# Kernel optimization log

Measured on AMD Instinct MI355X. Metric: run time of the kernel, lower is better.

The kernel has to match this reference:

```python
import jax, jax.numpy as jnp
import numpy as np

B, D, H, W, K = 2, 128, 256, 256, 4
OFFSET_SCALE = 1.0
BN_EPS = 1e-5


def conv2d(x, w, b=None, pad='SAME'):
    y = jax.lax.conv_general_dilated(x, w, (1, 1), pad,
                                     dimension_numbers=('NCHW', 'OIHW', 'NCHW'))
    if b is not None:
        y = y + b[None, :, None, None]
    return y


def grid_sample_border(img, gx, gy):
    # img: (b,d,H,W); gx,gy: (b,K,H,W) normalized coords in [-1,1]
    # bilinear, padding_mode='border', align_corners=True
    b, d, h, w = img.shape
    x = jnp.clip((gx + 1.0) * 0.5 * (w - 1), 0.0, w - 1)
    y = jnp.clip((gy + 1.0) * 0.5 * (h - 1), 0.0, h - 1)
    x0f = jnp.floor(x); y0f = jnp.floor(y)
    wx = x - x0f; wy = y - y0f
    x0 = x0f.astype(jnp.int32); y0 = y0f.astype(jnp.int32)
    x1 = jnp.minimum(x0 + 1, w - 1); y1 = jnp.minimum(y0 + 1, h - 1)
    imgT = jnp.transpose(img, (0, 2, 3, 1))  # (b,H,W,d)
    bidx = jnp.arange(b)[:, None, None, None]  # broadcasts over (b,K,H,W)
    def gather(yi, xi):
        return imgT[bidx, yi, xi]  # (b,K,H,W,d)
    out = (gather(y0, x0) * ((1 - wx) * (1 - wy))[..., None]
           + gather(y0, x1) * (wx * (1 - wy))[..., None]
           + gather(y1, x0) * ((1 - wx) * wy)[..., None]
           + gather(y1, x1) * (wx * wy)[..., None])
    return out  # (b,K,H,W,d)


def setup_inputs() -> dict:
    key = jax.random.key(0)
    ks = jax.random.split(key, 6)
    return {
        'bev': jax.random.normal(ks[0], (B, D, H, W), jnp.float32),
        'offset_w': jax.random.normal(ks[1], (2 * K, D, 3, 3), jnp.float32) * 0.02,
        'offset_b': jax.random.normal(ks[2], (2 * K,), jnp.float32) * 0.02,
        'weight_w': jax.random.normal(ks[3], (K, D, 3, 3), jnp.float32) * 0.05,
        'weight_b': jnp.zeros((K,), jnp.float32),
        'proj_w': jax.random.normal(ks[4], (D, D, 1, 1), jnp.float32) * (1.0 / np.sqrt(D)),
        'bn_gamma': jnp.ones((D,), jnp.float32),
        'bn_beta': jnp.zeros((D,), jnp.float32),
    }


def reference(bev, offset_w, offset_b, weight_w, weight_b, proj_w, bn_gamma, bn_beta):
    b, d, h, w = bev.shape
    # per-pixel K offsets (pixels) and K attention weights
    offsets = conv2d(bev, offset_w, offset_b) * OFFSET_SCALE  # (b,2K,H,W)
    w_logits = conv2d(bev, weight_w, weight_b)                # (b,K,H,W)
    attn = jax.nn.softmax(w_logits, axis=1)                   # softmax over K
    # base grid: replicates torch meshgrid(xy) + transpose (requires H==W)
    xs = jnp.linspace(-1.0, 1.0, w)
    ys = jnp.linspace(-1.0, 1.0, h)
    base_x = xs[:, None] * jnp.ones((1, h), jnp.float32)  # base_x[i,j] = xs[i]
    base_y = jnp.ones((w, 1), jnp.float32) * ys[None, :]  # base_y[i,j] = ys[j]
    off = offsets.reshape(b, K, 2, h, w)
    dx = off[:, :, 0]  # (b,K,H,W)
    dy = off[:, :, 1]
    dx_n = dx * (2.0 / (w - 1)) if w > 1 else dx * 0.0
    dy_n = dy * (2.0 / (h - 1)) if h > 1 else dy * 0.0
    gx = base_x[None, None] + dx_n  # (b,K,H,W)
    gy = base_y[None, None] + dy_n
    sampled = grid_sample_border(bev, gx, gy)  # (b,K,H,W,d)
    aggregated = jnp.einsum('bkhwd,bkhw->bdhw', sampled, attn)
    # proj: 1x1 conv (no bias) + BatchNorm2d (training mode: batch stats) + GELU(exact)
    y = conv2d(aggregated, proj_w)
    mean = jnp.mean(y, axis=(0, 2, 3), keepdims=True)
    var = jnp.mean((y - mean) ** 2, axis=(0, 2, 3), keepdims=True)
    y = (y - mean) * jax.lax.rsqrt(var + BN_EPS)
    y = y * bn_gamma[None, :, None, None] + bn_beta[None, :, None, None]
    return jax.nn.gelu(y, approximate=False)
```

## Files before the change

kernel.cpp:

```cpp
#include <hip/hip_runtime.h>
#include <math.h>

#define BB 2
#define DD 128
#define HH 256
#define WW 256
#define KK 4
#define HWC (HH*WW)
#define SROW2 320

typedef unsigned int u32;
typedef unsigned short ushort;
typedef __attribute__((ext_vector_type(8))) short bf16x8;
typedef __attribute__((ext_vector_type(4))) float f32x4;

#define OA_OFF    0
#define WTT_OFF   1572864
#define WP_OFF    1589248
#define STATS_OFF 1603072
#define PART_OFF  1603392
#define BEVT_OFF  1605440
#define PACC_OFF  18382656
#define PART2_OFF PACC_OFF
#define WBF_OFF   26771264
#define WCB_OFF   26779456
#define WS_NEED_BEVT  ((size_t)PACC_OFF * 4)
#define WS_NEED_FULL3 ((size_t)(WCB_OFF + 9216) * 4)

__device__ __forceinline__ u32 f2bf(float x) {
    u32 u = __builtin_bit_cast(u32, x);
    return (u + 0x7fffu + ((u >> 16) & 1u)) >> 16;
}
__device__ __forceinline__ u32 pkbf(float a, float b) {
    return f2bf(a) | (f2bf(b) << 16);
}
__device__ __forceinline__ float bflo(u32 d) { return __builtin_bit_cast(float, d << 16); }
__device__ __forceinline__ float bfhi(u32 d) { return __builtin_bit_cast(float, d & 0xffff0000u); }

__global__ __launch_bounds__(256) void k0_prep(
    const float* __restrict__ projw, const float* __restrict__ offw,
    const float* __restrict__ wtw, float* __restrict__ wtT, float* __restrict__ wp)
{
    int idx = blockIdx.x * 256 + threadIdx.x;
    if (idx < 16384) {
        int d = idx >> 7, o = idx & 127;
        wtT[d * 128 + o] = projw[o * 128 + d];
    }
    if (idx < 13824) {
        int c = idx / 108; int r = idx % 108; int o = r / 9; int t = r % 9;
        wp[idx] = (o < 8) ? offw[(o*128 + c)*9 + t] : wtw[((o-8)*128 + c)*9 + t];
    }
}

__global__ __launch_bounds__(256) void k0bc(
    const float* __restrict__ projw, const float* __restrict__ offw,
    const float* __restrict__ wtw, ushort* __restrict__ wbf,
    ushort* __restrict__ wcb)
{
    int idx = blockIdx.x * 256 + threadIdx.x;
    if (idx < 16384) wbf[idx] = (ushort)f2bf(projw[idx]);
    if (idx < 18432) {
        int tap = idx >> 11;
        int rem = idx & 2047;
        int oo = rem >> 7, c = rem & 127;
        float v = 0.f;
        if (oo < 8)       v = offw[(oo*128 + c)*9 + tap];
        else if (oo < 12) v = wtw[((oo-8)*128 + c)*9 + tap];
        wcb[idx] = (ushort)f2bf(v);
    }
}

__global__ __launch_bounds__(256) void k2t_bf(
    const float* __restrict__ bev, ushort* __restrict__ bevtb)
{
    __shared__ float T[64 * 128];
    int tid = threadIdx.x;
    int bidx = blockIdx.x;
    int b = bidx >> 10;
    int rem = bidx & 1023;
    int yrow = rem >> 2;
    int x0 = (rem & 3) << 6;

    const float* src = bev + ((size_t)b * DD) * HWC + (size_t)yrow * WW + x0;
    #pragma unroll 4
    for (int k = 0; k < 32; k++) {
        int flat = k * 256 + tid;
        int d = flat >> 6, xl = flat & 63;
        float v = src[(size_t)d * HWC + xl];
        T[xl * 128 + (((d >> 2) ^ (xl & 31)) << 2) + (d & 3)] = v;
    }
    __syncthreads();
    ushort* dst = bevtb + (((size_t)b * HH + yrow) * WW + x0) * 128;
    #pragma unroll 4
    for (int k = 0; k < 8; k++) {
        int flat = k * 256 + tid;
        int d4 = flat & 31, xl = (flat >> 5) & 63;
        float4 v = *(const float4*)&T[xl * 128 + ((d4 ^ (xl & 31)) << 2)];
        uint2 pk;
        pk.x = pkbf(v.x, v.y);
        pk.y = pkbf(v.z, v.w);
        *(uint2*)(dst + (size_t)xl * 128 + (d4 << 2)) = pk;
    }
}

__global__ __launch_bounds__(128) void k1m_conv_mfma(
    const ushort* __restrict__ bevtb, const ushort* __restrict__ wcb,
    const float* __restrict__ offb, const float* __restrict__ wtb,
    float* __restrict__ oa)
{
    __shared__ uint4 lds4[1632];

    int tid = threadIdx.x;
    int wv = tid >> 6;
    int l = tid & 63;
    int lm = l & 15, lk = l >> 4;
    int wgid = blockIdx.x;
    int lin = (wgid & 7) * 512 + (wgid >> 3);
    int b = lin >> 11;
    int i = (lin >> 3) & 255;
    int jt = lin & 7;
    int x0 = jt * 32;

    const ushort* bb = bevtb + (size_t)b * HWC * 128;
    for (int z = tid; z < 1632; z += 128) {
        int row = z / 544;
        int rem = z - row * 544;
        int pl = rem >> 4;
        int q  = rem & 15;
        int yy = i - 1 + row;
        int x  = x0 - 1 + pl;
        bool ok = ((unsigned)yy < HH) && ((unsigned)x < WW);
        uint4 v = make_uint4(0u, 0u, 0u, 0u);
        if (ok) v = *(const uint4*)(bb + ((size_t)(yy * WW + x) << 7) + q * 8);
        lds4[row * 544 + pl * 16 + (q ^ (pl & 15))] = v;
    }
    __syncthreads();

    f32x4 acc = (f32x4)(0.f);
    #pragma unroll
    for (int dy = 0; dy < 3; dy++) {
        #pragma unroll
        for (int dx = 0; dx < 3; dx++) {
            int pl = wv * 16 + lm + dx;
            const uint4* bp = &lds4[dy * 544 + pl * 16];
            int sx = pl & 15;
            const ushort* ap = wcb + (size_t)((dy*3 + dx) * 16 + lm) * 128 + lk * 8;
            #pragma unroll
            for (int kk = 0; kk < 4; kk++) {
                bf16x8 bfr = *(const bf16x8*)&bp[(kk*4 + lk) ^ sx];
                bf16x8 afr = *(const bf16x8*)(ap + kk * 32);
                acc = __builtin_amdgcn_mfma_f32_16x16x32_bf16(afr, bfr, acc, 0, 0, 0);
            }
        }
    }

    float v[4];
    #pragma unroll
    for (int r = 0; r < 4; r++) v[r] = acc[r];

    int j = x0 + wv * 16 + lm;
    if (lk < 2) {
        #pragma unroll
        for (int r = 0; r < 4; r++) v[r] += offb[lk*4 + r];
    } else if (lk == 2) {
        float l4[4];
        #pragma unroll
        for (int r = 0; r < 4; r++) l4[r] = v[r] + wtb[r];
        float m = fmaxf(fmaxf(l4[0], l4[1]), fmaxf(l4[2], l4[3]));
        float e[4]; float se = 0.f;
        #pragma unroll
        for (int r = 0; r < 4; r++) { e[r] = expf(l4[r] - m); se += e[r]; }
        float inv = 1.f / se;
        #pragma unroll
        for (int r = 0; r < 4; r++) v[r] = e[r] * inv;
    }
    if (lk < 3) {
        size_t basep = (size_t)b * 12 * HWC + (size_t)i * WW + j;
        #pragma unroll
        for (int r = 0; r < 4; r++)
            oa[basep + (size_t)(lk*4 + r) * HWC] = v[r];
    }
}

#define TAPPTR(t) (bt + ((size_t)((((t) & 1) ? (pa[(t) >> 1] >> 16) : (pa[(t) >> 1] & 0xffffu))) << 7))
#define FMA8(S, V, W) do { \
    S[0] = fmaf(W, bflo((V).x), S[0]); S[1] = fmaf(W, bfhi((V).x), S[1]); \
    S[2] = fmaf(W, bflo((V).y), S[2]); S[3] = fmaf(W, bfhi((V).y), S[3]); \
    S[4] = fmaf(W, bflo((V).z), S[4]); S[5] = fmaf(W, bfhi((V).z), S[5]); \
    S[6] = fmaf(W, bflo((V).w), S[6]); S[7] = fmaf(W, bfhi((V).w), S[7]); \
} while (0)

__global__ __launch_bounds__(256, 4) void k2f_sample_proj(
    const ushort* __restrict__ bevtb, const float* __restrict__ oa,
    const ushort* __restrict__ wbf, float* __restrict__ y,
    float* __restrict__ part2)
{
    __shared__ uint4 P[32 * 16];

    int tid = threadIdx.x;
    int wgid = blockIdx.x;
    int lin = (wgid & 7) * 512 + (wgid >> 3);
    int b = lin >> 11;
    int pix0 = (lin & 2047) << 5;

    int q8 = tid & 7;
    int pixl = tid >> 3;
    int pix = pix0 + pixl;
    int p = pix >> 8;
    int q = pix & 255;

    const float* ob = oa + (size_t)b * 12 * HWC + (size_t)p * WW + q;
    unsigned pa[8]; float cw[16];
    #pragma unroll
    for (int k = 0; k < 4; k++) {
        float dx = ob[(size_t)(2*k)   * HWC];
        float dy = ob[(size_t)(2*k+1) * HWC];
        float a  = ob[(size_t)(8+k)   * HWC];
        float x  = fminf(fmaxf((float)p + dx, 0.f), (float)(WW-1));
        float yv = fminf(fmaxf((float)q + dy, 0.f), (float)(HH-1));
        float x0f = floorf(x); float y0f = floorf(yv);
        int x0 = (int)x0f; int y0 = (int)y0f;
        int x1 = min(x0 + 1, WW - 1); int y1 = min(y0 + 1, HH - 1);
        float wx = x - x0f; float wy = yv - y0f;
        pa[k*2+0] = (unsigned)(y0*WW + x0) | ((unsigned)(y0*WW + x1) << 16);
        pa[k*2+1] = (unsigned)(y1*WW + x0) | ((unsigned)(y1*WW + x1) << 16);
        cw[k*4+0] = a * (1.f - wx) * (1.f - wy);
        cw[k*4+1] = a * wx * (1.f - wy);
        cw[k*4+2] = a * (1.f - wx) * wy;
        cw[k*4+3] = a * wx * wy;
    }

    const ushort* bt = bevtb + (size_t)b * HWC * 128 + q8 * 8;

    float s[2][8];
    #pragma unroll
    for (int c = 0; c < 2; c++)
        #pragma unroll
        for (int e = 0; e < 8; e++) s[c][e] = 0.f;

    uint4 L0[8], L1[8];
    #pragma unroll
    for (int t = 0; t < 8; t++) L0[t] = *(const uint4*)(TAPPTR(t));
    #pragma unroll
    for (int t = 0; t < 8; t++) L1[t] = *(const uint4*)(TAPPTR(t + 8));
    #pragma unroll
    for (int t = 0; t < 8; t++) {
        uint4 v = L0[t];
        L0[t] = *(const uint4*)(TAPPTR(t) + 64);
        FMA8(s[0], v, cw[t]);
    }
    #pragma unroll
    for (int t = 0; t < 8; t++) {
        uint4 v = L1[t];
        L1[t] = *(const uint4*)(TAPPTR(t + 8) + 64);
        FMA8(s[0], v, cw[t + 8]);
    }
    #pragma unroll
    for (int t = 0; t < 8; t++) FMA8(s[1], L0[t], cw[t]);
    #pragma unroll
    for (int t = 0; t < 8; t++) FMA8(s[1], L1[t], cw[t + 8]);

    int sxr = pixl & 15;
    #pragma unroll
    for (int c = 0; c < 2; c++) {
        uint4 pk;
        pk.x = pkbf(s[c][0], s[c][1]);
        pk.y = pkbf(s[c][2], s[c][3]);
        pk.z = pkbf(s[c][4], s[c][5]);
        pk.w = pkbf(s[c][6], s[c][7]);
        P[pixl * 16 + ((c * 8 + q8) ^ sxr)] = pk;
    }
    __syncthreads();

    int wv = tid >> 6;
    int l = tid & 63;
    int lm = l & 15, lk = l >> 4;
    int o0 = wv << 5;

    f32x4 acc[2][2];
    #pragma unroll
    for (int ot = 0; ot < 2; ot++)
        #pragma unroll
        for (int nt = 0; nt < 2; nt++)
            acc[ot][nt] = (f32x4)(0.f);

    #pragma unroll
    for (int ot = 0; ot < 2; ot++) {
        const ushort* ap = wbf + (size_t)(o0 + ot * 16 + lm) * 128 + lk * 8;
        bf16x8 a4[4];
        #pragma unroll
        for (int kk = 0; kk < 4; kk++)
            a4[kk] = *(const bf16x8*)(ap + kk * 32);
        #pragma unroll
        for (int nt = 0; nt < 2; nt++) {
            int row = nt * 16 + lm;
            #pragma unroll
            for (int kk = 0; kk < 4; kk++) {
                bf16x8 bfr = *(const bf16x8*)&P[row * 16 + ((kk * 4 + lk) ^ lm)];
                acc[ot][nt] = __builtin_amdgcn_mfma_f32_16x16x32_bf16(
                    a4[kk], bfr, acc[ot][nt], 0, 0, 0);
            }
        }
    }

    #pragma unroll
    for (int ot = 0; ot < 2; ot++)
        #pragma unroll
        for (int nt = 0; nt < 2; nt++)
            #pragma unroll
            for (int r = 0; r < 4; r++)
                y[((size_t)b * DD + o0 + ot * 16 + lk * 4 + r) * HWC + pix0 + nt * 16 + lm]
                    = acc[ot][nt][r];

    float sm[2][4], sq[2][4];
    #pragma unroll
    for (int ot = 0; ot < 2; ot++)
        #pragma unroll
        for (int r = 0; r < 4; r++) { sm[ot][r] = 0.f; sq[ot][r] = 0.f; }
    #pragma unroll
    for (int ot = 0; ot < 2; ot++)
        #pragma unroll
        for (int nt = 0; nt < 2; nt++)
            #pragma unroll
            for (int r = 0; r < 4; r++) {
                float v = acc[ot][nt][r];
                sm[ot][r] += v;
                sq[ot][r] = fmaf(v, v, sq[ot][r]);
            }
    #pragma unroll
    for (int m = 1; m < 16; m <<= 1) {
        #pragma unroll
        for (int ot = 0; ot < 2; ot++)
            #pragma unroll
            for (int r = 0; r < 4; r++) {
                sm[ot][r] += __shfl_xor(sm[ot][r], m);
                sq[ot][r] += __shfl_xor(sq[ot][r], m);
            }
    }
    if (lm == 0) {
        float* pw = part2 + (size_t)wgid * 256;
        #pragma unroll
        for (int ot = 0; ot < 2; ot++)
            #pragma unroll
            for (int r = 0; r < 4; r++) {
                int o = o0 + ot * 16 + lk * 4 + r;
                pw[o] = sm[ot][r];
                pw[128 + o] = sq[ot][r];
            }
    }
}

__global__ __launch_bounds__(256) void k3b_finalize2(
    const float* __restrict__ part2, const float* __restrict__ gamma,
    const float* __restrict__ beta, float* __restrict__ stats)
{
    int o = blockIdx.x; int tid = threadIdx.x;
    double s = 0.0, s2 = 0.0;
    for (int w = tid; w < 4096; w += 256) {
        s  += (double)part2[(size_t)w * 256 + o];
        s2 += (double)part2[(size_t)w * 256 + 128 + o];
    }
    __shared__ double ls[256], ls2[256];
    ls[tid] = s; ls2[tid] = s2;
    __syncthreads();
    for (int off = 128; off > 0; off >>= 1) {
        if (tid < off) { ls[tid] += ls[tid+off]; ls2[tid] += ls2[tid+off]; }
        __syncthreads();
    }
    if (tid == 0) {
        double N = (double)(BB * HWC);
        double mean = ls[0] / N;
        double var = ls2[0] / N - mean * mean;
        double invs = 1.0 / sqrt(var + 1e-5);
        double g = (double)gamma[o];
        stats[o*2]   = (float)(g * invs);
        stats[o*2+1] = (float)((double)beta[o] - mean * g * invs);
    }
}

__global__ __launch_bounds__(256) void k1_convs(
    const float* __restrict__ bev, const float* __restrict__ wp,
    const float* __restrict__ offb, const float* __restrict__ wtb,
    float* __restrict__ oa)
{
    __shared__ float rows[2][3][260];
    int tid = threadIdx.x;
    int p = blockIdx.x;
    int b = p / HH; int i = p % HH; int j = tid;
    const float* bb = bev + (size_t)b * DD * HWC;

    if (tid < 12) { int bf = tid / 6, r = tid % 6; rows[bf][r >> 1][(r & 1) ? 257 : 0] = 0.f; }
    #pragma unroll
    for (int l = 0; l < 3; l++) {
        int yy = i + l - 1;
        rows[0][l][1 + tid] = ((unsigned)yy < HH) ? bb[yy * WW + tid] : 0.f;
    }
    __syncthreads();

    float acc[12];
    #pragma unroll
    for (int o = 0; o < 12; o++) acc[o] = 0.f;

    for (int c = 0; c < 128; c++) {
        int cb = c & 1, nb = cb ^ 1;
        float rv[3];
        if (c < 127) {
            const float* pln = bb + (size_t)(c + 1) * HWC;
            #pragma unroll
            for (int l = 0; l < 3; l++) {
                int yy = i + l - 1;
                rv[l] = ((unsigned)yy < HH) ? pln[yy * WW + tid] : 0.f;
            }
        }
        float v[9];
        #pragma unroll
        for (int dy = 0; dy < 3; dy++)
            #pragma unroll
            for (int dx = 0; dx < 3; dx++)
                v[dy*3 + dx] = rows[cb][dy][tid + dx];
        const float* wc = wp + c * 108;
        #pragma unroll
        for (int o = 0; o < 12; o++) {
            float s = acc[o];
            #pragma unroll
            for (int t = 0; t < 9; t++) s = fmaf(wc[o*9 + t], v[t], s);
            acc[o] = s;
        }
        if (c < 127) {
            #pragma unroll
            for (int l = 0; l < 3; l++) rows[nb][l][1 + tid] = rv[l];
        }
        __syncthreads();
    }

    float outv[12];
    #pragma unroll
    for (int o = 0; o < 8; o++) outv[o] = acc[o] + offb[o];
    float l4[4];
    #pragma unroll
    for (int k = 0; k < 4; k++) l4[k] = acc[8+k] + wtb[k];
    float m = fmaxf(fmaxf(l4[0], l4[1]), fmaxf(l4[2], l4[3]));
    float e[4]; float se = 0.f;
    #pragma unroll
    for (int k = 0; k < 4; k++) { e[k] = expf(l4[k] - m); se += e[k]; }
    float inv = 1.f / se;
    #pragma unroll
    for (int k = 0; k < 4; k++) outv[8+k] = e[k] * inv;

    size_t basep = (size_t)b * 12 * HWC + (size_t)i * WW + j;
    #pragma unroll
    for (int o = 0; o < 12; o++) oa[basep + (size_t)o * HWC] = outv[o];
}

__global__ __launch_bounds__(256) void k2t_transpose(
    const float* __restrict__ bev, float* __restrict__ bevt)
{
    __shared__ float T[64 * 128];
    int tid = threadIdx.x;
    int bidx = blockIdx.x;
    int b = bidx >> 10;
    int rem = bidx & 1023;
    int yrow = rem >> 2;
    int x0 = (rem & 3) << 6;

    const float* src = bev + ((size_t)b * DD) * HWC + (size_t)yrow * WW + x0;
    #pragma unroll 4
    for (int k = 0; k < 32; k++) {
        int flat = k * 256 + tid;
        int d = flat >> 6, xl = flat & 63;
        float v = src[(size_t)d * HWC + xl];
        T[xl * 128 + (((d >> 2) ^ (xl & 31)) << 2) + (d & 3)] = v;
    }
    __syncthreads();
    float* dst = bevt + (((size_t)b * HH + yrow) * WW + x0) * 128;
    #pragma unroll 4
    for (int k = 0; k < 8; k++) {
        int flat = k * 256 + tid;
        int d4 = flat & 31, xl = (flat >> 5) & 63;
        float4 v = *(const float4*)&T[xl * 128 + ((d4 ^ (xl & 31)) << 2)];
        *(float4*)(dst + (size_t)xl * 128 + (d4 << 2)) = v;
    }
}

__global__ __launch_bounds__(512, 2) void k2_sample_proj_t(
    const float* __restrict__ bevt, const float* __restrict__ oa,
    const float* __restrict__ wt, float* __restrict__ y)
{
    __shared__ float S[2][16 * SROW2];

    int tid = threadIdx.x;
    int bidx = blockIdx.x;
    int b  = bidx >> 8;
    int p0 = ((bidx >> 4) & 15) * 16;
    int q0 = (bidx & 15) * 16;

    int gpix = tid >> 1;
    int gp = gpix & 15;
    int gq = gpix >> 4;
    int dgrp = tid & 1;
    int swr = gp * 20 + gq;

    int wv = tid >> 6;
    int wvu = __builtin_amdgcn_readfirstlane(wv);
    int lane = tid & 63;
    int lp = lane >> 2;
    int q4 = (lane & 3) << 2;
    int soff = lp * 20 + q4;

    const float* ob = oa + (size_t)b * 12 * HWC + (size_t)(p0 + gp) * WW + (q0 + gq);
    unsigned pa[8]; float cw[16];
    #pragma unroll
    for (int k = 0; k < 4; k++) {
        float dx = ob[(size_t)(2*k)   * HWC];
        float dy = ob[(size_t)(2*k+1) * HWC];
        float a  = ob[(size_t)(8+k)   * HWC];
        float x  = fminf(fmaxf((float)(p0 + gp) + dx, 0.f), (float)(WW-1));
        float yv = fminf(fmaxf((float)(q0 + gq) + dy, 0.f), (float)(HH-1));
        float x0f = floorf(x); float y0f = floorf(yv);
        int x0 = (int)x0f; int y0 = (int)y0f;
        int x1 = min(x0 + 1, WW - 1); int y1 = min(y0 + 1, HH - 1);
        float wx = x - x0f; float wy = yv - y0f;
        pa[k*2+0] = (unsigned)(y0*WW + x0) | ((unsigned)(y0*WW + x1) << 16);
        pa[k*2+1] = (unsigned)(y1*WW + x0) | ((unsigned)(y1*WW + x1) << 16);
        cw[k*4+0] = a * (1.f - wx) * (1.f - wy);
        cw[k*4+1] = a * wx * (1.f - wy);
        cw[k*4+2] = a * (1.f - wx) * wy;
        cw[k*4+3] = a * wx * wy;
    }

    const float* bt = bevt + (size_t)b * HWC * 128 + dgrp * 8;

    float acc[64];
    #pragma unroll
    for (int t = 0; t < 64; t++) acc[t] = 0.f;

    {
        float4 s0 = make_float4(0,0,0,0), s1 = make_float4(0,0,0,0);
        #pragma unroll
        for (int t = 0; t < 16; t++) {
            unsigned pix = (t & 1) ? (pa[t >> 1] >> 16) : (pa[t >> 1] & 0xffffu);
            const float4* tp = (const float4*)(bt + ((size_t)pix << 7));
            float4 va = tp[0], vb = tp[1];
            float c = cw[t];
            s0.x = fmaf(c, va.x, s0.x); s0.y = fmaf(c, va.y, s0.y);
            s0.z = fmaf(c, va.z, s0.z); s0.w = fmaf(c, va.w, s0.w);
            s1.x = fmaf(c, vb.x, s1.x); s1.y = fmaf(c, vb.y, s1.y);
            s1.z = fmaf(c, vb.z, s1.z); s1.w = fmaf(c, vb.w, s1.w);
        }
        int r = dgrp * 8;
        S[0][(r+0)*SROW2 + swr] = s0.x; S[0][(r+1)*SROW2 + swr] = s0.y;
        S[0][(r+2)*SROW2 + swr] = s0.z; S[0][(r+3)*SROW2 + swr] = s0.w;
        S[0][(r+4)*SROW2 + swr] = s1.x; S[0][(r+5)*SROW2 + swr] = s1.y;
        S[0][(r+6)*SROW2 + swr] = s1.z; S[0][(r+7)*SROW2 + swr] = s1.w;
    }
    __syncthreads();

    for (int c = 0; c < 8; c++) {
        int cur = c & 1;
        const float* Sc = &S[cur][0];
        float* Sn = &S[cur ^ 1][0];
        int d0 = c * 16;
        int dn = d0 + 16;
        bool more = (c < 7);

        float4 g0 = make_float4(0,0,0,0), g1 = make_float4(0,0,0,0);
        float4 pf0, pf1;
        if (more) {
            unsigned pix = pa[0] & 0xffffu;
            const float4* tp = (const float4*)(bt + ((size_t)pix << 7) + dn);
            pf0 = tp[0]; pf1 = tp[1];
        }

        #pragma unroll
        for (int dl = 0; dl < 16; dl++) {
            float4 cur0 = pf0, cur1 = pf1;
            if (more && dl < 15) {
                int t = dl + 1;
                unsigned pix = (t & 1) ? (pa[t >> 1] >> 16) : (pa[t >> 1] & 0xffffu);
                const float4* tp = (const float4*)(bt + ((size_t)pix << 7) + dn);
                pf0 = tp[0]; pf1 = tp[1];
            }

            float4 sv = *(const float4*)(Sc + dl * SROW2 + soff);
            const float4* wq = (const float4*)(wt + (size_t)(d0 + dl) * 128 + wvu * 16);
            #pragma unroll
            for (int oi4 = 0; oi4 < 4; oi4++) {
                float4 w4 = wq[oi4];
                int ob4 = oi4 * 16;
                acc[ob4+ 0] = fmaf(w4.x, sv.x, acc[ob4+ 0]);
                acc[ob4+ 1] = fmaf(w4.x, sv.y, acc[ob4+ 1]);
                acc[ob4+ 2] = fmaf(w4.x, sv.z, acc[ob4+ 2]);
                acc[ob4+ 3] = fmaf(w4.x, sv.w, acc[ob4+ 3]);
                acc[ob4+ 4] = fmaf(w4.y, sv.x, acc[ob4+ 4]);
                acc[ob4+ 5] = fmaf(w4.y, sv.y, acc[ob4+ 5]);
                acc[ob4+ 6] = fmaf(w4.y, sv.z, acc[ob4+ 6]);
                acc[ob4+ 7] = fmaf(w4.y, sv.w, acc[ob4+ 7]);
                acc[ob4+ 8] = fmaf(w4.z, sv.x, acc[ob4+ 8]);
                acc[ob4+ 9] = fmaf(w4.z, sv.y, acc[ob4+ 9]);
                acc[ob4+10] = fmaf(w4.z, sv.z, acc[ob4+10]);
                acc[ob4+11] = fmaf(w4.z, sv.w, acc[ob4+11]);
                acc[ob4+12] = fmaf(w4.w, sv.x, acc[ob4+12]);
                acc[ob4+13] = fmaf(w4.w, sv.y, acc[ob4+13]);
                acc[ob4+14] = fmaf(w4.w, sv.z, acc[ob4+14]);
                acc[ob4+15] = fmaf(w4.w, sv.w, acc[ob4+15]);
            }

            if (more) {
                float cwt = cw[dl];
                g0.x = fmaf(cwt, cur0.x, g0.x); g0.y = fmaf(cwt, cur0.y, g0.y);
                g0.z = fmaf(cwt, cur0.z, g0.z); g0.w = fmaf(cwt, cur0.w, g0.w);
                g1.x = fmaf(cwt, cur1.x, g1.x); g1.y = fmaf(cwt, cur1.y, g1.y);
                g1.z = fmaf(cwt, cur1.z, g1.z); g1.w = fmaf(cwt, cur1.w, g1.w);
            }
        }

        if (more) {
            int r = dgrp * 8;
            Sn[(r+0)*SROW2 + swr] = g0.x; Sn[(r+1)*SROW2 + swr] = g0.y;
            Sn[(r+2)*SROW2 + swr] = g0.z; Sn[(r+3)*SROW2 + swr] = g0.w;
            Sn[(r+4)*SROW2 + swr] = g1.x; Sn[(r+5)*SROW2 + swr] = g1.y;
            Sn[(r+6)*SROW2 + swr] = g1.z; Sn[(r+7)*SROW2 + swr] = g1.w;
        }
        __syncthreads();
    }

    size_t base = (size_t)b * DD * HWC + (size_t)(p0 + lp) * WW + (q0 + q4);
    #pragma unroll
    for (int oi = 0; oi < 16; oi++) {
        int o = wv * 16 + oi;
        float4 v = make_float4(acc[oi*4+0], acc[oi*4+1], acc[oi*4+2], acc[oi*4+3]);
        *(float4*)(y + base + (size_t)o * HWC) = v;
    }
}

__global__ __launch_bounds__(512, 2) void k2_sample_proj(
    const float* __restrict__ bev, const float* __restrict__ oa,
    const float* __restrict__ wt, float* __restrict__ y)
{
    __shared__ float S[2][16 * SROW2];
    int tid = threadIdx.x;
    int bidx = blockIdx.x;
    int b  = bidx >> 8;
    int p0 = ((bidx >> 4) & 15) * 16;
    int q0 = (bidx & 15) * 16;
    int pix = tid & 255;
    int gq = pix >> 4;
    int gp = pix & 15;
    int dgrp = tid >> 8;
    int swr = gp * 20 + gq;
    int wv = tid >> 6;
    int wvu = __builtin_amdgcn_readfirstlane(wv);
    int lane = tid & 63;
    int lp = lane >> 2;
    int q4 = (lane & 3) << 2;
    int soff = lp * 20 + q4;

    const float* ob = oa + (size_t)b * 12 * HWC + (size_t)(p0 + gp) * WW + (q0 + gq);
    unsigned pa[8]; float cw[16];
    #pragma unroll
    for (int k = 0; k < 4; k++) {
        float dx = ob[(size_t)(2*k)   * HWC];
        float dy = ob[(size_t)(2*k+1) * HWC];
        float a  = ob[(size_t)(8+k)   * HWC];
        float x  = fminf(fmaxf((float)(p0 + gp) + dx, 0.f), (float)(WW-1));
        float yv = fminf(fmaxf((float)(q0 + gq) + dy, 0.f), (float)(HH-1));
        float x0f = floorf(x); float y0f = floorf(yv);
        int x0 = (int)x0f; int y0 = (int)y0f;
        int x1 = min(x0 + 1, WW - 1); int y1 = min(y0 + 1, HH - 1);
        float wx = x - x0f; float wy = yv - y0f;
        pa[k*2+0] = (unsigned)(y0*WW + x0) | ((unsigned)(y0*WW + x1) << 16);
        pa[k*2+1] = (unsigned)(y1*WW + x0) | ((unsigned)(y1*WW + x1) << 16);
        cw[k*4+0] = a * (1.f - wx) * (1.f - wy);
        cw[k*4+1] = a * wx * (1.f - wy);
        cw[k*4+2] = a * (1.f - wx) * wy;
        cw[k*4+3] = a * wx * wy;
    }
    const float* bb = bev + (size_t)b * DD * HWC;
    float acc[64];
    #pragma unroll
    for (int t = 0; t < 64; t++) acc[t] = 0.f;
    #pragma unroll
    for (int dd = 0; dd < 8; dd++) {
        const float* pl = bb + (size_t)(dgrp*8 + dd) * HWC;
        float s = 0.f;
        #pragma unroll
        for (int t = 0; t < 8; t++) {
            unsigned a01 = pa[t];
            s = fmaf(cw[2*t],   pl[a01 & 0xffffu], s);
            s = fmaf(cw[2*t+1], pl[a01 >> 16], s);
        }
        S[0][(dgrp*8 + dd) * SROW2 + swr] = s;
    }
    __syncthreads();
    for (int c = 0; c < 8; c++) {
        int cur = c & 1;
        const float* Sc = &S[cur][0];
        float* Sn = &S[cur ^ 1][0];
        int d0 = c * 16;
        int d0n = d0 + 16;
        bool more = (c < 7);
        #pragma unroll
        for (int dl = 0; dl < 16; dl++) {
            if (dl < 8) {
                if (more) {
                    const float* pl = bb + (size_t)(d0n + dgrp*8 + dl) * HWC;
                    float s = 0.f;
                    #pragma unroll
                    for (int t = 0; t < 8; t++) {
                        unsigned a01 = pa[t];
                        s = fmaf(cw[2*t],   pl[a01 & 0xffffu], s);
                        s = fmaf(cw[2*t+1], pl[a01 >> 16], s);
                    }
                    Sn[(dgrp*8 + dl) * SROW2 + swr] = s;
                }
            }
            float4 sv = *(const float4*)(Sc + dl * SROW2 + soff);
            const float4* wq = (const float4*)(wt + (size_t)(d0 + dl) * 128 + wvu * 16);
            #pragma unroll
            for (int oi4 = 0; oi4 < 4; oi4++) {
                float4 w4 = wq[oi4];
                int ob4 = oi4 * 16;
                acc[ob4+ 0] = fmaf(w4.x, sv.x, acc[ob4+ 0]);
                acc[ob4+ 1] = fmaf(w4.x, sv.y, acc[ob4+ 1]);
                acc[ob4+ 2] = fmaf(w4.x, sv.z, acc[ob4+ 2]);
                acc[ob4+ 3] = fmaf(w4.x, sv.w, acc[ob4+ 3]);
                acc[ob4+ 4] = fmaf(w4.y, sv.x, acc[ob4+ 4]);
                acc[ob4+ 5] = fmaf(w4.y, sv.y, acc[ob4+ 5]);
                acc[ob4+ 6] = fmaf(w4.y, sv.z, acc[ob4+ 6]);
                acc[ob4+ 7] = fmaf(w4.y, sv.w, acc[ob4+ 7]);
                acc[ob4+ 8] = fmaf(w4.z, sv.x, acc[ob4+ 8]);
                acc[ob4+ 9] = fmaf(w4.z, sv.y, acc[ob4+ 9]);
                acc[ob4+10] = fmaf(w4.z, sv.z, acc[ob4+10]);
                acc[ob4+11] = fmaf(w4.z, sv.w, acc[ob4+11]);
                acc[ob4+12] = fmaf(w4.w, sv.x, acc[ob4+12]);
                acc[ob4+13] = fmaf(w4.w, sv.y, acc[ob4+13]);
                acc[ob4+14] = fmaf(w4.w, sv.z, acc[ob4+14]);
                acc[ob4+15] = fmaf(w4.w, sv.w, acc[ob4+15]);
            }
        }
        __syncthreads();
    }
    size_t base = (size_t)b * DD * HWC + (size_t)(p0 + lp) * WW + (q0 + q4);
    #pragma unroll
    for (int oi = 0; oi < 16; oi++) {
        int o = wv * 16 + oi;
        float4 v = make_float4(acc[oi*4+0], acc[oi*4+1], acc[oi*4+2], acc[oi*4+3]);
        *(float4*)(y + base + (size_t)o * HWC) = v;
    }
}

__global__ __launch_bounds__(256) void k3_partial(
    const float* __restrict__ y, double* __restrict__ part)
{
    int blk = blockIdx.x;
    int o = blk >> 2; int sub = blk & 3; int b = sub >> 1; int half = sub & 1;
    const float4* pl = (const float4*)(y + ((size_t)b * DD + o) * HWC + half * (HWC/2));
    int tid = threadIdx.x;
    double s = 0.0, s2 = 0.0;
    for (int idx = tid; idx < HWC/8; idx += 256) {
        float4 v = pl[idx];
        s  += (double)v.x + (double)v.y + (double)v.z + (double)v.w;
        s2 += (double)v.x*v.x + (double)v.y*v.y + (double)v.z*v.z + (double)v.w*v.w;
    }
    __shared__ double ls[256], ls2[256];
    ls[tid] = s; ls2[tid] = s2;
    __syncthreads();
    for (int off = 128; off > 0; off >>= 1) {
        if (tid < off) { ls[tid] += ls[tid+off]; ls2[tid] += ls2[tid+off]; }
        __syncthreads();
    }
    if (tid == 0) { part[blk*2] = ls[0]; part[blk*2+1] = ls2[0]; }
}

__global__ __launch_bounds__(128) void k3_finalize(
    const double* __restrict__ part, const float* __restrict__ gamma,
    const float* __restrict__ beta, float* __restrict__ stats)
{
    int o = threadIdx.x;
    double s = 0.0, s2 = 0.0;
    #pragma unroll
    for (int j = 0; j < 4; j++) { s += part[(o*4+j)*2]; s2 += part[(o*4+j)*2+1]; }
    double N = (double)(BB * HWC);
    double mean = s / N;
    double var = s2 / N - mean * mean;
    double invs = 1.0 / sqrt(var + 1e-5);
    double g = (double)gamma[o];
    stats[o*2]   = (float)(g * invs);
    stats[o*2+1] = (float)((double)beta[o] - mean * g * invs);
}

__global__ __launch_bounds__(256) void k4_bn_gelu(
    float* __restrict__ y, const float* __restrict__ stats)
{
    size_t idx4 = (size_t)blockIdx.x * 256 + threadIdx.x;
    float4* p = (float4*)y;
    float4 v = p[idx4];
    int o = (int)((idx4 * 4) / HWC) % DD;
    float sc = stats[o*2], sh = stats[o*2+1];
    const float inv_sqrt2 = 0.70710678118654752f;
    float g0 = fmaf(v.x, sc, sh);
    float g1 = fmaf(v.y, sc, sh);
    float g2 = fmaf(v.z, sc, sh);
    float g3 = fmaf(v.w, sc, sh);
    v.x = 0.5f * g0 * (1.f + erff(g0 * inv_sqrt2));
    v.y = 0.5f * g1 * (1.f + erff(g1 * inv_sqrt2));
    v.z = 0.5f * g2 * (1.f + erff(g2 * inv_sqrt2));
    v.w = 0.5f * g3 * (1.f + erff(g3 * inv_sqrt2));
    p[idx4] = v;
}

extern "C" void kernel_launch(void* const* d_in, const int* in_sizes, int n_in,
                              void* d_out, int out_size, void* d_ws, size_t ws_size,
                              hipStream_t stream) {
    const float* bev   = (const float*)d_in[0];
    const float* offw  = (const float*)d_in[1];
    const float* offb  = (const float*)d_in[2];
    const float* wtw   = (const float*)d_in[3];
    const float* wtb   = (const float*)d_in[4];
    const float* projw = (const float*)d_in[5];
    const float* gamma = (const float*)d_in[6];
    const float* beta  = (const float*)d_in[7];
    float* out = (float*)d_out;
    float* wsf = (float*)d_ws;

    float* oa    = wsf + OA_OFF;
    float* wtT   = wsf + WTT_OFF;
    float* wp    = wsf + WP_OFF;
    float* stats = wsf + STATS_OFF;
    double* part = (double*)(wsf + PART_OFF);
    float* bevt  = wsf + BEVT_OFF;
    ushort* bevtb = (ushort*)(wsf + BEVT_OFF);
    ushort* wbf  = (ushort*)(wsf + WBF_OFF);
    ushort* wcb  = (ushort*)(wsf + WCB_OFF);
    float* part2 = wsf + PART2_OFF;

    bool full3 = ws_size >= WS_NEED_FULL3;
    bool big   = ws_size >= WS_NEED_BEVT;

    if (full3) {
        hipLaunchKernelGGL(k0bc, dim3(72), dim3(256), 0, stream,
                           projw, offw, wtw, wbf, wcb);
        hipLaunchKernelGGL(k2t_bf, dim3(2048), dim3(256), 0, stream, bev, bevtb);
        hipLaunchKernelGGL(k1m_conv_mfma, dim3(4096), dim3(128), 0, stream,
                           bevtb, wcb, offb, wtb, oa);
        hipLaunchKernelGGL(k2f_sample_proj, dim3(4096), dim3(256), 0, stream,
                           bevtb, oa, wbf, out, part2);
        hipLaunchKernelGGL(k3b_finalize2, dim3(128), dim3(256), 0, stream,
                           part2, gamma, beta, stats);
    } else if (big) {
        hipLaunchKernelGGL(k0_prep, dim3(64), dim3(256), 0, stream,
                           projw, offw, wtw, wtT, wp);
        hipLaunchKernelGGL(k2t_transpose, dim3(2048), dim3(256), 0, stream, bev, bevt);
        hipLaunchKernelGGL(k1_convs, dim3(BB*HH), dim3(256), 0, stream,
                           bev, wp, offb, wtb, oa);
        hipLaunchKernelGGL(k2_sample_proj_t, dim3(BB*256), dim3(512), 0, stream,
                           bevt, oa, wtT, out);
        hipLaunchKernelGGL(k3_partial, dim3(512), dim3(256), 0, stream, out, part);
        hipLaunchKernelGGL(k3_finalize, dim3(1), dim3(128), 0, stream,
                           part, gamma, beta, stats);
    } else {
        hipLaunchKernelGGL(k0_prep, dim3(64), dim3(256), 0, stream,
                           projw, offw, wtw, wtT, wp);
        hipLaunchKernelGGL(k1_convs, dim3(BB*HH), dim3(256), 0, stream,
                           bev, wp, offb, wtb, oa);
        hipLaunchKernelGGL(k2_sample_proj, dim3(BB*256), dim3(512), 0, stream,
                           bev, oa, wtT, out);
        hipLaunchKernelGGL(k3_partial, dim3(512), dim3(256), 0, stream, out, part);
        hipLaunchKernelGGL(k3_finalize, dim3(1), dim3(128), 0, stream,
                           part, gamma, beta, stats);
    }
    hipLaunchKernelGGL(k4_bn_gelu, dim3((BB*DD*HWC)/1024), dim3(256), 0, stream,
                       out, stats);
}
```

Baseline: 156.3 us.

## Store pre-BN projection in bf16 and widen conv tiles to 64 pixels

The sample-projection kernel now writes its pre-BatchNorm output as bf16 into a workspace buffer, and a new BN+GELU kernel reads it in bf16 and writes fp32 output. This halves the write and read traffic of the 16M-element intermediate. The MFMA offset/weight conv kernel now uses 256-thread blocks covering 64 pixels per row, which reuses the halo more and halves the block count. The intermediate fp32 path is also removed. Rounding y to bf16 adds error before normalization, while the batch statistics still come from fp32 accumulators.

```diff
diff --git a/kernel.cpp b/kernel.cpp
--- a/kernel.cpp
+++ b/kernel.cpp
@@ -20,6 +20,7 @@
 #define STATS_OFF 1603072
 #define PART_OFF  1603392
 #define BEVT_OFF  1605440
+#define YBF_OFF   9994048
 #define PACC_OFF  18382656
 #define PART2_OFF PACC_OFF
 #define WBF_OFF   26771264
@@ -103,28 +104,28 @@
     }
 }
 
-__global__ __launch_bounds__(128) void k1m_conv_mfma(
+__global__ __launch_bounds__(256) void k1m_conv_mfma(
     const ushort* __restrict__ bevtb, const ushort* __restrict__ wcb,
     const float* __restrict__ offb, const float* __restrict__ wtb,
     float* __restrict__ oa)
 {
-    __shared__ uint4 lds4[1632];
+    __shared__ uint4 lds4[3168];
 
     int tid = threadIdx.x;
     int wv = tid >> 6;
     int l = tid & 63;
     int lm = l & 15, lk = l >> 4;
     int wgid = blockIdx.x;
-    int lin = (wgid & 7) * 512 + (wgid >> 3);
-    int b = lin >> 11;
-    int i = (lin >> 3) & 255;
-    int jt = lin & 7;
-    int x0 = jt * 32;
+    int lin = (wgid & 7) * 256 + (wgid >> 3);
+    int b = lin >> 10;
+    int i = (lin >> 2) & 255;
+    int jt = lin & 3;
+    int x0 = jt * 64;
 
     const ushort* bb = bevtb + (size_t)b * HWC * 128;
-    for (int z = tid; z < 1632; z += 128) {
-        int row = z / 544;
-        int rem = z - row * 544;
+    for (int z = tid; z < 3168; z += 256) {
+        int row = z / 1056;
+        int rem = z - row * 1056;
         int pl = rem >> 4;
         int q  = rem & 15;
         int yy = i - 1 + row;
@@ -132,7 +133,7 @@
         bool ok = ((unsigned)yy < HH) && ((unsigned)x < WW);
         uint4 v = make_uint4(0u, 0u, 0u, 0u);
         if (ok) v = *(const uint4*)(bb + ((size_t)(yy * WW + x) << 7) + q * 8);
-        lds4[row * 544 + pl * 16 + (q ^ (pl & 15))] = v;
+        lds4[row * 1056 + pl * 16 + (q ^ (pl & 15))] = v;
     }
     __syncthreads();
 
@@ -142,7 +143,7 @@
         #pragma unroll
         for (int dx = 0; dx < 3; dx++) {
             int pl = wv * 16 + lm + dx;
-            const uint4* bp = &lds4[dy * 544 + pl * 16];
+            const uint4* bp = &lds4[dy * 1056 + pl * 16];
             int sx = pl & 15;
             const ushort* ap = wcb + (size_t)((dy*3 + dx) * 16 + lm) * 128 + lk * 8;
             #pragma unroll
@@ -192,7 +193,7 @@
 
 __global__ __launch_bounds__(256, 4) void k2f_sample_proj(
     const ushort* __restrict__ bevtb, const float* __restrict__ oa,
-    const ushort* __restrict__ wbf, float* __restrict__ y,
+    const ushort* __restrict__ wbf, ushort* __restrict__ ybf,
     float* __restrict__ part2)
 {
     __shared__ uint4 P[32 * 16];
@@ -309,8 +310,8 @@
         for (int nt = 0; nt < 2; nt++)
             #pragma unroll
             for (int r = 0; r < 4; r++)
-                y[((size_t)b * DD + o0 + ot * 16 + lk * 4 + r) * HWC + pix0 + nt * 16 + lm]
-                    = acc[ot][nt][r];
+                ybf[((size_t)b * DD + o0 + ot * 16 + lk * 4 + r) * HWC + pix0 + nt * 16 + lm]
+                    = (ushort)f2bf(acc[ot][nt][r]);
 
     float sm[2][4], sq[2][4];
     #pragma unroll
@@ -378,6 +379,33 @@
     }
 }
 
+__global__ __launch_bounds__(256) void k4_bn_gelu_bf(
+    const ushort* __restrict__ ybf, const float* __restrict__ stats,
+    float* __restrict__ out)
+{
+    size_t idx8 = (size_t)blockIdx.x * 256 + threadIdx.x;
+    uint4 v = ((const uint4*)ybf)[idx8];
+    int o = (int)((idx8 * 8) / HWC) % DD;
+    float sc = stats[o*2], sh = stats[o*2+1];
+    const float is2 = 0.70710678118654752f;
+    float g[8];
+    g[0] = fmaf(bflo(v.x), sc, sh); g[1] = fmaf(bfhi(v.x), sc, sh);
+    g[2] = fmaf(bflo(v.y), sc, sh); g[3] = fmaf(bfhi(v.y), sc, sh);
+    g[4] = fmaf(bflo(v.z), sc, sh); g[5] = fmaf(bfhi(v.z), sc, sh);
+    g[6] = fmaf(bflo(v.w), sc, sh); g[7] = fmaf(bfhi(v.w), sc, sh);
+    float4 o0, o1;
+    o0.x = 0.5f * g[0] * (1.f + erff(g[0] * is2));
+    o0.y = 0.5f * g[1] * (1.f + erff(g[1] * is2));
+    o0.z = 0.5f * g[2] * (1.f + erff(g[2] * is2));
+    o0.w = 0.5f * g[3] * (1.f + erff(g[3] * is2));
+    o1.x = 0.5f * g[4] * (1.f + erff(g[4] * is2));
+    o1.y = 0.5f * g[5] * (1.f + erff(g[5] * is2));
+    o1.z = 0.5f * g[6] * (1.f + erff(g[6] * is2));
+    o1.w = 0.5f * g[7] * (1.f + erff(g[7] * is2));
+    ((float4*)out)[idx8 * 2]     = o0;
+    ((float4*)out)[idx8 * 2 + 1] = o1;
+}
+
 __global__ __launch_bounds__(256) void k1_convs(
     const float* __restrict__ bev, const float* __restrict__ wp,
     const float* __restrict__ offb, const float* __restrict__ wtb,
@@ -450,187 +478,6 @@
     size_t basep = (size_t)b * 12 * HWC + (size_t)i * WW + j;
     #pragma unroll
     for (int o = 0; o < 12; o++) oa[basep + (size_t)o * HWC] = outv[o];
-}
-
-__global__ __launch_bounds__(256) void k2t_transpose(
-    const float* __restrict__ bev, float* __restrict__ bevt)
-{
-    __shared__ float T[64 * 128];
-    int tid = threadIdx.x;
-    int bidx = blockIdx.x;
-    int b = bidx >> 10;
-    int rem = bidx & 1023;
-    int yrow = rem >> 2;
-    int x0 = (rem & 3) << 6;
-
-    const float* src = bev + ((size_t)b * DD) * HWC + (size_t)yrow * WW + x0;
-    #pragma unroll 4
-    for (int k = 0; k < 32; k++) {
-        int flat = k * 256 + tid;
-        int d = flat >> 6, xl = flat & 63;
-        float v = src[(size_t)d * HWC + xl];
-        T[xl * 128 + (((d >> 2) ^ (xl & 31)) << 2) + (d & 3)] = v;
-    }
-    __syncthreads();
-    float* dst = bevt + (((size_t)b * HH + yrow) * WW + x0) * 128;
-    #pragma unroll 4
-    for (int k = 0; k < 8; k++) {
-        int flat = k * 256 + tid;
-        int d4 = flat & 31, xl = (flat >> 5) & 63;
-        float4 v = *(const float4*)&T[xl * 128 + ((d4 ^ (xl & 31)) << 2)];
-        *(float4*)(dst + (size_t)xl * 128 + (d4 << 2)) = v;
-    }
-}
-
-__global__ __launch_bounds__(512, 2) void k2_sample_proj_t(
-    const float* __restrict__ bevt, const float* __restrict__ oa,
-    const float* __restrict__ wt, float* __restrict__ y)
-{
-    __shared__ float S[2][16 * SROW2];
-
-    int tid = threadIdx.x;
-    int bidx = blockIdx.x;
-    int b  = bidx >> 8;
-    int p0 = ((bidx >> 4) & 15) * 16;
-    int q0 = (bidx & 15) * 16;
-
-    int gpix = tid >> 1;
-    int gp = gpix & 15;
-    int gq = gpix >> 4;
-    int dgrp = tid & 1;
-    int swr = gp * 20 + gq;
-
-    int wv = tid >> 6;
-    int wvu = __builtin_amdgcn_readfirstlane(wv);
-    int lane = tid & 63;
-    int lp = lane >> 2;
-    int q4 = (lane & 3) << 2;
-    int soff = lp * 20 + q4;
-
-    const float* ob = oa + (size_t)b * 12 * HWC + (size_t)(p0 + gp) * WW + (q0 + gq);
-    unsigned pa[8]; float cw[16];
-    #pragma unroll
-    for (int k = 0; k < 4; k++) {
-        float dx = ob[(size_t)(2*k)   * HWC];
-        float dy = ob[(size_t)(2*k+1) * HWC];
-        float a  = ob[(size_t)(8+k)   * HWC];
-        float x  = fminf(fmaxf((float)(p0 + gp) + dx, 0.f), (float)(WW-1));
-        float yv = fminf(fmaxf((float)(q0 + gq) + dy, 0.f), (float)(HH-1));
-        float x0f = floorf(x); float y0f = floorf(yv);
-        int x0 = (int)x0f; int y0 = (int)y0f;
-        int x1 = min(x0 + 1, WW - 1); int y1 = min(y0 + 1, HH - 1);
-        float wx = x - x0f; float wy = yv - y0f;
-        pa[k*2+0] = (unsigned)(y0*WW + x0) | ((unsigned)(y0*WW + x1) << 16);
-        pa[k*2+1] = (unsigned)(y1*WW + x0) | ((unsigned)(y1*WW + x1) << 16);
-        cw[k*4+0] = a * (1.f - wx) * (1.f - wy);
-        cw[k*4+1] = a * wx * (1.f - wy);
-        cw[k*4+2] = a * (1.f - wx) * wy;
-        cw[k*4+3] = a * wx * wy;
-    }
-
-    const float* bt = bevt + (size_t)b * HWC * 128 + dgrp * 8;
-
-    float acc[64];
-    #pragma unroll
-    for (int t = 0; t < 64; t++) acc[t] = 0.f;
-
-    {
-        float4 s0 = make_float4(0,0,0,0), s1 = make_float4(0,0,0,0);
-        #pragma unroll
-        for (int t = 0; t < 16; t++) {
-            unsigned pix = (t & 1) ? (pa[t >> 1] >> 16) : (pa[t >> 1] & 0xffffu);
-            const float4* tp = (const float4*)(bt + ((size_t)pix << 7));
-            float4 va = tp[0], vb = tp[1];
-            float c = cw[t];
-            s0.x = fmaf(c, va.x, s0.x); s0.y = fmaf(c, va.y, s0.y);
-            s0.z = fmaf(c, va.z, s0.z); s0.w = fmaf(c, va.w, s0.w);
-            s1.x = fmaf(c, vb.x, s1.x); s1.y = fmaf(c, vb.y, s1.y);
-            s1.z = fmaf(c, vb.z, s1.z); s1.w = fmaf(c, vb.w, s1.w);
-        }
-        int r = dgrp * 8;
-        S[0][(r+0)*SROW2 + swr] = s0.x; S[0][(r+1)*SROW2 + swr] = s0.y;
-        S[0][(r+2)*SROW2 + swr] = s0.z; S[0][(r+3)*SROW2 + swr] = s0.w;
-        S[0][(r+4)*SROW2 + swr] = s1.x; S[0][(r+5)*SROW2 + swr] = s1.y;
-        S[0][(r+6)*SROW2 + swr] = s1.z; S[0][(r+7)*SROW2 + swr] = s1.w;
-    }
-    __syncthreads();
-
-    for (int c = 0; c < 8; c++) {
-        int cur = c & 1;
-        const float* Sc = &S[cur][0];
-        float* Sn = &S[cur ^ 1][0];
-        int d0 = c * 16;
-        int dn = d0 + 16;
-        bool more = (c < 7);
-
-        float4 g0 = make_float4(0,0,0,0), g1 = make_float4(0,0,0,0);
-        float4 pf0, pf1;
-        if (more) {
-            unsigned pix = pa[0] & 0xffffu;
-            const float4* tp = (const float4*)(bt + ((size_t)pix << 7) + dn);
-            pf0 = tp[0]; pf1 = tp[1];
-        }
-
-        #pragma unroll
-        for (int dl = 0; dl < 16; dl++) {
-            float4 cur0 = pf0, cur1 = pf1;
-            if (more && dl < 15) {
-                int t = dl + 1;
-                unsigned pix = (t & 1) ? (pa[t >> 1] >> 16) : (pa[t >> 1] & 0xffffu);
-                const float4* tp = (const float4*)(bt + ((size_t)pix << 7) + dn);
-                pf0 = tp[0]; pf1 = tp[1];
-            }
-
-            float4 sv = *(const float4*)(Sc + dl * SROW2 + soff);
-            const float4* wq = (const float4*)(wt + (size_t)(d0 + dl) * 128 + wvu * 16);
-            #pragma unroll
-            for (int oi4 = 0; oi4 < 4; oi4++) {
-                float4 w4 = wq[oi4];
-                int ob4 = oi4 * 16;
-                acc[ob4+ 0] = fmaf(w4.x, sv.x, acc[ob4+ 0]);
-                acc[ob4+ 1] = fmaf(w4.x, sv.y, acc[ob4+ 1]);
-                acc[ob4+ 2] = fmaf(w4.x, sv.z, acc[ob4+ 2]);
-                acc[ob4+ 3] = fmaf(w4.x, sv.w, acc[ob4+ 3]);
-                acc[ob4+ 4] = fmaf(w4.y, sv.x, acc[ob4+ 4]);
-                acc[ob4+ 5] = fmaf(w4.y, sv.y, acc[ob4+ 5]);
-                acc[ob4+ 6] = fmaf(w4.y, sv.z, acc[ob4+ 6]);
-                acc[ob4+ 7] = fmaf(w4.y, sv.w, acc[ob4+ 7]);
-                acc[ob4+ 8] = fmaf(w4.z, sv.x, acc[ob4+ 8]);
-                acc[ob4+ 9] = fmaf(w4.z, sv.y, acc[ob4+ 9]);
-                acc[ob4+10] = fmaf(w4.z, sv.z, acc[ob4+10]);
-                acc[ob4+11] = fmaf(w4.z, sv.w, acc[ob4+11]);
-                acc[ob4+12] = fmaf(w4.w, sv.x, acc[ob4+12]);
-                acc[ob4+13] = fmaf(w4.w, sv.y, acc[ob4+13]);
-                acc[ob4+14] = fmaf(w4.w, sv.z, acc[ob4+14]);
-                acc[ob4+15] = fmaf(w4.w, sv.w, acc[ob4+15]);
-            }
-
-            if (more) {
-                float cwt = cw[dl];
-                g0.x = fmaf(cwt, cur0.x, g0.x); g0.y = fmaf(cwt, cur0.y, g0.y);
-                g0.z = fmaf(cwt, cur0.z, g0.z); g0.w = fmaf(cwt, cur0.w, g0.w);
-                g1.x = fmaf(cwt, cur1.x, g1.x); g1.y = fmaf(cwt, cur1.y, g1.y);
-                g1.z = fmaf(cwt, cur1.z, g1.z); g1.w = fmaf(cwt, cur1.w, g1.w);
-            }
-        }
-
-        if (more) {
-            int r = dgrp * 8;
-            Sn[(r+0)*SROW2 + swr] = g0.x; Sn[(r+1)*SROW2 + swr] = g0.y;
-            Sn[(r+2)*SROW2 + swr] = g0.z; Sn[(r+3)*SROW2 + swr] = g0.w;
-            Sn[(r+4)*SROW2 + swr] = g1.x; Sn[(r+5)*SROW2 + swr] = g1.y;
-            Sn[(r+6)*SROW2 + swr] = g1.z; Sn[(r+7)*SROW2 + swr] = g1.w;
-        }
-        __syncthreads();
-    }
-
-    size_t base = (size_t)b * DD * HWC + (size_t)(p0 + lp) * WW + (q0 + q4);
-    #pragma unroll
-    for (int oi = 0; oi < 16; oi++) {
-        int o = wv * 16 + oi;
-        float4 v = make_float4(acc[oi*4+0], acc[oi*4+1], acc[oi*4+2], acc[oi*4+3]);
-        *(float4*)(y + base + (size_t)o * HWC) = v;
-    }
 }
 
 __global__ __launch_bounds__(512, 2) void k2_sample_proj(
@@ -828,36 +675,26 @@
     float* wp    = wsf + WP_OFF;
     float* stats = wsf + STATS_OFF;
     double* part = (double*)(wsf + PART_OFF);
-    float* bevt  = wsf + BEVT_OFF;
     ushort* bevtb = (ushort*)(wsf + BEVT_OFF);
+    ushort* ybf   = (ushort*)(wsf + YBF_OFF);
     ushort* wbf  = (ushort*)(wsf + WBF_OFF);
     ushort* wcb  = (ushort*)(wsf + WCB_OFF);
     float* part2 = wsf + PART2_OFF;
 
     bool full3 = ws_size >= WS_NEED_FULL3;
-    bool big   = ws_size >= WS_NEED_BEVT;
 
     if (full3) {
         hipLaunchKernelGGL(k0bc, dim3(72), dim3(256), 0, stream,
                            projw, offw, wtw, wbf, wcb);
         hipLaunchKernelGGL(k2t_bf, dim3(2048), dim3(256), 0, stream, bev, bevtb);
-        hipLaunchKernelGGL(k1m_conv_mfma, dim3(4096), dim3(128), 0, stream,
+        hipLaunchKernelGGL(k1m_conv_mfma, dim3(2048), dim3(256), 0, stream,
                            bevtb, wcb, offb, wtb, oa);
         hipLaunchKernelGGL(k2f_sample_proj, dim3(4096), dim3(256), 0, stream,
-                           bevtb, oa, wbf, out, part2);
+                           bevtb, oa, wbf, ybf, part2);
         hipLaunchKernelGGL(k3b_finalize2, dim3(128), dim3(256), 0, stream,
                            part2, gamma, beta, stats);
-    } else if (big) {
-        hipLaunchKernelGGL(k0_prep, dim3(64), dim3(256), 0, stream,
-                           projw, offw, wtw, wtT, wp);
-        hipLaunchKernelGGL(k2t_transpose, dim3(2048), dim3(256), 0, stream, bev, bevt);
-        hipLaunchKernelGGL(k1_convs, dim3(BB*HH), dim3(256), 0, stream,
-                           bev, wp, offb, wtb, oa);
-        hipLaunchKernelGGL(k2_sample_proj_t, dim3(BB*256), dim3(512), 0, stream,
-                           bevt, oa, wtT, out);
-        hipLaunchKernelGGL(k3_partial, dim3(512), dim3(256), 0, stream, out, part);
-        hipLaunchKernelGGL(k3_finalize, dim3(1), dim3(128), 0, stream,
-                           part, gamma, beta, stats);
+        hipLaunchKernelGGL(k4_bn_gelu_bf, dim3((BB*DD*HWC)/2048), dim3(256), 0, stream,
+                           ybf, stats, out);
     } else {
         hipLaunchKernelGGL(k0_prep, dim3(64), dim3(256), 0, stream,
                            projw, offw, wtw, wtT, wp);
@@ -868,7 +705,7 @@
         hipLaunchKernelGGL(k3_partial, dim3(512), dim3(256), 0, stream, out, part);
         hipLaunchKernelGGL(k3_finalize, dim3(1), dim3(128), 0, stream,
                            part, gamma, beta, stats);
-    }
-    hipLaunchKernelGGL(k4_bn_gelu, dim3((BB*DD*HWC)/1024), dim3(256), 0, stream,
-                       out, stats);
-}
+        hipLaunchKernelGGL(k4_bn_gelu, dim3((BB*DD*HWC)/1024), dim3(256), 0, stream,
+                           out, stats);
+    }
+}
```

Result: faster. 151.3 us (-3.2%).
